# Kernel optimization log

Measured on AMD Instinct MI355X. Metric: run time of the kernel, lower is better.

## Reference

```python
import jax, jax.numpy as jnp
import numpy as np

NUM_HEADS = 16


def setup_inputs() -> dict:
    key = jax.random.key(0)
    ks = jax.random.split(key, 11)
    S, E, F = 4096, 2048, 8192
    s = lambda k, shape, fan_in: jax.random.normal(k, shape, jnp.float32) / np.sqrt(fan_in)
    return {
        "emb": jax.random.normal(ks[0], (S, E), jnp.float32),
        "Wq": s(ks[1], (E, E), E), "bq": jnp.zeros((E,), jnp.float32),
        "Wk": s(ks[2], (E, E), E), "bk": jnp.zeros((E,), jnp.float32),
        "Wv": s(ks[3], (E, E), E), "bv": jnp.zeros((E,), jnp.float32),
        "W1": s(ks[4], (E, F), E), "b1": jnp.zeros((F,), jnp.float32),
        "W2": s(ks[5], (F, E), F), "b2": jnp.zeros((E,), jnp.float32),
    }


def reference(emb, Wq, bq, Wk, bk, Wv, bv, W1, b1, W2, b2):
    S, E = emb.shape
    H = NUM_HEADS
    D = E // H
    # project and split heads -> [H, S, D]
    q = (emb @ Wq + bq).reshape(S, H, D).transpose(1, 0, 2)
    k = (emb @ Wk + bk).reshape(S, H, D).transpose(1, 0, 2)
    v = (emb @ Wv + bv).reshape(S, H, D).transpose(1, 0, 2)
    scale = jnp.asarray(D, emb.dtype) ** 0.5
    scores = jnp.einsum("hsd,htd->hst", q, k) / scale  # [H, S, S]
    # causal mask: additive -1e9 strictly above the diagonal (matches torch.triu(..., 1)*-1e9)
    mask = jnp.triu(jnp.full((S, S), -1e9, dtype=scores.dtype), k=1)
    probs = jax.nn.softmax(scores + mask, axis=-1)
    attn = jnp.einsum("hst,htd->hsd", probs, v)  # [H, S, D]
    attn = attn.transpose(1, 0, 2).reshape(S, E)  # concat heads -> [S, E]
    hidden = jnp.maximum(attn @ W1 + b1, 0.0)
    return hidden @ W2 + b2
```

## Files before the change

### kernel.cpp

```cpp
#include <hip/hip_runtime.h>

typedef __attribute__((ext_vector_type(8))) short bf16x8;
typedef __attribute__((ext_vector_type(4))) float f32x4;
typedef __attribute__((ext_vector_type(8))) unsigned short u16x8;

static constexpr int S = 4096;
static constexpr int E = 2048;
static constexpr int F = 8192;
static constexpr int NH = 16;
static constexpr int DH = 128;

__device__ __forceinline__ unsigned short f2bf(float f) {
  unsigned u = __builtin_bit_cast(unsigned, f);
  u += 0x7FFFu + ((u >> 16) & 1u);
  return (unsigned short)(u >> 16);
}

__device__ __forceinline__ void async16(const unsigned short* g, unsigned short* l) {
  __builtin_amdgcn_global_load_lds(
      (const __attribute__((address_space(1))) unsigned int*)g,
      (__attribute__((address_space(3))) unsigned int*)l, 16, 0, 0);
}

__global__ __launch_bounds__(256) void cvt_bf16_kernel(const float* __restrict__ src,
                                                       unsigned short* __restrict__ dst) {
  int i = (blockIdx.x * 256 + threadIdx.x) * 4;
  float4 v = *(const float4*)(src + i);
  ushort4 o;
  o.x = f2bf(v.x); o.y = f2bf(v.y); o.z = f2bf(v.z); o.w = f2bf(v.w);
  *(ushort4*)(dst + i) = o;
}

__global__ __launch_bounds__(256) void transpose_cvt(const float* __restrict__ src,
                                                     unsigned short* __restrict__ dst,
                                                     const int Rr, const int Cc) {
  __shared__ float t[32][33];
  const int c0 = blockIdx.x * 32, r0 = blockIdx.y * 32;
  const int tx = threadIdx.x, ty = threadIdx.y;
#pragma unroll
  for (int i = 0; i < 4; ++i) {
    int r = ty + i * 8;
    t[r][tx] = src[(size_t)(r0 + r) * Cc + c0 + tx];
  }
  __syncthreads();
#pragma unroll
  for (int i = 0; i < 4; ++i) {
    int cr = ty + i * 8;
    dst[(size_t)(c0 + cr) * Rr + r0 + tx] = f2bf(t[tx][cr]);
  }
}

enum { EPI_QKV = 0, EPI_RELU = 1, EPI_OUT = 2 };

template <int EPI>
__global__ __launch_bounds__(256) void gemm_bt(
    const unsigned short* __restrict__ A, const unsigned short* __restrict__ B,
    const int K, const int N,
    const float* __restrict__ b0, const float* __restrict__ b1f, const float* __restrict__ b2f,
    unsigned short* __restrict__ o0, unsigned short* __restrict__ o1,
    unsigned short* __restrict__ o2, float* __restrict__ of) {
  __shared__ unsigned short lA[2][128 * 32];
  __shared__ unsigned short lB[2][128 * 32];
  const int tid = threadIdx.x, w = tid >> 6, lane = tid & 63;
  const int lane15 = lane & 15, l4 = lane >> 4;
  const int m0 = blockIdx.y * 128, n0 = blockIdx.x * 128;
  const int wr = w >> 1, wc = w & 1;

  const int u0 = (w * 2 + 0) * 64 + lane;
  const int u1 = (w * 2 + 1) * 64 + lane;
  const unsigned short* gA0 = A + (size_t)(m0 + (u0 >> 2)) * K + (u0 & 3) * 8;
  const unsigned short* gA1 = A + (size_t)(m0 + (u1 >> 2)) * K + (u1 & 3) * 8;
  const unsigned short* gB0 = B + (size_t)(n0 + (u0 >> 2)) * K + (u0 & 3) * 8;
  const unsigned short* gB1 = B + (size_t)(n0 + (u1 >> 2)) * K + (u1 & 3) * 8;
  const int doff0 = (w * 2 + 0) * 512;
  const int doff1 = (w * 2 + 1) * 512;

  f32x4 zero4 = {0.f, 0.f, 0.f, 0.f};
  f32x4 acc[4][4];
#pragma unroll
  for (int i = 0; i < 4; ++i)
#pragma unroll
    for (int j = 0; j < 4; ++j) acc[i][j] = zero4;

  async16(gA0, &lA[0][doff0]);
  async16(gA1, &lA[0][doff1]);
  async16(gB0, &lB[0][doff0]);
  async16(gB1, &lB[0][doff1]);

  for (int ko = 0; ko < K; ko += 32) {
    __syncthreads();
    const int buf = (ko >> 5) & 1;
    if (ko + 32 < K) {
      const int nb = buf ^ 1;
      async16(gA0 + ko + 32, &lA[nb][doff0]);
      async16(gA1 + ko + 32, &lA[nb][doff1]);
      async16(gB0 + ko + 32, &lB[nb][doff0]);
      async16(gB1 + ko + 32, &lB[nb][doff1]);
    }
    bf16x8 av[4], bv[4];
#pragma unroll
    for (int i = 0; i < 4; ++i)
      av[i] = *(const bf16x8*)&lA[buf][(wr * 64 + i * 16 + lane15) * 32 + l4 * 8];
#pragma unroll
    for (int j = 0; j < 4; ++j)
      bv[j] = *(const bf16x8*)&lB[buf][(wc * 64 + j * 16 + lane15) * 32 + l4 * 8];
#pragma unroll
    for (int i = 0; i < 4; ++i)
#pragma unroll
      for (int j = 0; j < 4; ++j)
        acc[i][j] = __builtin_amdgcn_mfma_f32_16x16x32_bf16(av[i], bv[j], acc[i][j], 0, 0, 0);
  }

#pragma unroll
  for (int j = 0; j < 4; ++j) {
    const int n = n0 + wc * 64 + j * 16 + lane15;
    float bias;
    if (EPI == EPI_QKV)
      bias = (n < E) ? b0[n] : ((n < 2 * E) ? b1f[n - E] : b2f[n - 2 * E]);
    else
      bias = b0[n];
#pragma unroll
    for (int i = 0; i < 4; ++i) {
      const int mr = m0 + wr * 64 + i * 16 + l4 * 4;
      f32x4 v = acc[i][j];
#pragma unroll
      for (int r = 0; r < 4; ++r) {
        const float val = v[r] + bias;
        const int m = mr + r;
        if (EPI == EPI_QKV) {
          if (n < E)            o0[(size_t)m * E + n] = f2bf(val);
          else if (n < 2 * E)   o1[(size_t)m * E + (n - E)] = f2bf(val);
          else                  o2[(size_t)(n - 2 * E) * S + m] = f2bf(val);
        } else if (EPI == EPI_RELU) {
          o0[(size_t)m * N + n] = f2bf(fmaxf(val, 0.f));
        } else {
          of[(size_t)m * N + n] = val;
        }
      }
    }
  }
}

__global__ __launch_bounds__(256, 2) void flash_attn(const unsigned short* __restrict__ Qb,
                                                     const unsigned short* __restrict__ Kb,
                                                     const unsigned short* __restrict__ VTb,
                                                     unsigned short* __restrict__ attn) {
  const int qt = gridDim.x - 1 - blockIdx.x;
  const int h = blockIdx.y;
  const int qbase = qt * 64;
  const int tid = threadIdx.x, w = tid >> 6, lane = tid & 63;
  const int lane15 = lane & 15, l4 = lane >> 4;

  __shared__ unsigned short lK[2][64 * 128];
  __shared__ unsigned short lV[2][128 * 64];
  __shared__ unsigned short lP[4][16 * 72];

  bf16x8 aq[4];
  {
    const unsigned short* qrow = Qb + (size_t)(qbase + w * 16 + lane15) * E + h * DH + l4 * 8;
#pragma unroll
    for (int kk = 0; kk < 4; ++kk) aq[kk] = *(const bf16x8*)(qrow + kk * 32);
  }

  f32x4 zero4 = {0.f, 0.f, 0.f, 0.f};
  f32x4 o[8];
  float psum[4];
#pragma unroll
  for (int j = 0; j < 8; ++j) o[j] = zero4;
#pragma unroll
  for (int r = 0; r < 4; ++r) psum[r] = 0.f;

  {
#pragma unroll
    for (int i = 0; i < 4; ++i) {
      int c = i * 256 + w * 64 + lane;
      int row = c >> 4, pg = (c & 15) ^ (row & 15);
      async16(Kb + (size_t)row * E + h * DH + pg * 8, &lK[0][(i * 256 + w * 64) * 8]);
    }
#pragma unroll
    for (int i = 0; i < 4; ++i) {
      int c = i * 256 + w * 64 + lane;
      int row = c >> 3, pg = (c & 7) ^ (row & 7);
      async16(VTb + (size_t)(h * DH + row) * S + pg * 8, &lV[0][(i * 256 + w * 64) * 8]);
    }
  }

  const float scale = 0.088388347648318447f;

  for (int kt = 0; kt <= qt; ++kt) {
    __syncthreads();
    if (kt < qt) {
      const int kb2 = (kt + 1) * 64;
      const int nb = (kt + 1) & 1;
#pragma unroll
      for (int i = 0; i < 4; ++i) {
        int c = i * 256 + w * 64 + lane;
        int row = c >> 4, pg = (c & 15) ^ (row & 15);
        async16(Kb + (size_t)(kb2 + row) * E + h * DH + pg * 8, &lK[nb][(i * 256 + w * 64) * 8]);
      }
#pragma unroll
      for (int i = 0; i < 4; ++i) {
        int c = i * 256 + w * 64 + lane;
        int row = c >> 3, pg = (c & 7) ^ (row & 7);
        async16(VTb + (size_t)(h * DH + row) * S + kb2 + pg * 8, &lV[nb][(i * 256 + w * 64) * 8]);
      }
    }
    const int buf = kt & 1;

    f32x4 sacc[4];
#pragma unroll
    for (int j = 0; j < 4; ++j) sacc[j] = zero4;
#pragma unroll
    for (int kk = 0; kk < 4; ++kk)
#pragma unroll
      for (int j = 0; j < 4; ++j) {
        int pl = (kk * 4 + l4) ^ lane15;
        bf16x8 bk = *(const bf16x8*)&lK[buf][(j * 16 + lane15) * 128 + pl * 8];
        sacc[j] = __builtin_amdgcn_mfma_f32_16x16x32_bf16(aq[kk], bk, sacc[j], 0, 0, 0);
      }

    float p[4][4];
    if (kt == qt) {
#pragma unroll
      for (int j = 0; j < 4; ++j) {
        int col = j * 16 + lane15;
#pragma unroll
        for (int r = 0; r < 4; ++r) {
          int row = w * 16 + l4 * 4 + r;
          p[j][r] = (col <= row) ? __expf(sacc[j][r] * scale) : 0.f;
        }
      }
    } else {
#pragma unroll
      for (int j = 0; j < 4; ++j)
#pragma unroll
        for (int r = 0; r < 4; ++r) p[j][r] = __expf(sacc[j][r] * scale);
    }
#pragma unroll
    for (int r = 0; r < 4; ++r) psum[r] += p[0][r] + p[1][r] + p[2][r] + p[3][r];

#pragma unroll
    for (int j = 0; j < 4; ++j)
#pragma unroll
      for (int r = 0; r < 4; ++r)
        lP[w][(l4 * 4 + r) * 72 + j * 16 + lane15] = f2bf(p[j][r]);

#pragma unroll
    for (int ks = 0; ks < 2; ++ks) {
      bf16x8 ap = *(const bf16x8*)&lP[w][lane15 * 72 + ks * 32 + l4 * 8];
#pragma unroll
      for (int j = 0; j < 8; ++j) {
        int pl = (ks * 4 + l4) ^ (lane15 & 7);
        bf16x8 bv = *(const bf16x8*)&lV[buf][(j * 16 + lane15) * 64 + pl * 8];
        o[j] = __builtin_amdgcn_mfma_f32_16x16x32_bf16(ap, bv, o[j], 0, 0, 0);
      }
    }
  }

  float inv[4];
#pragma unroll
  for (int r = 0; r < 4; ++r) {
    float s = psum[r];
#pragma unroll
    for (int off = 1; off < 16; off <<= 1) s += __shfl_xor(s, off, 16);
    inv[r] = 1.0f / s;
  }
#pragma unroll
  for (int j = 0; j < 8; ++j)
#pragma unroll
    for (int r = 0; r < 4; ++r)
      attn[(size_t)(qbase + w * 16 + l4 * 4 + r) * E + h * DH + j * 16 + lane15] =
          f2bf(o[j][r] * inv[r]);
}

extern "C" void kernel_launch(void* const* d_in, const int* in_sizes, int n_in,
                              void* d_out, int out_size, void* d_ws, size_t ws_size,
                              hipStream_t stream) {
  (void)in_sizes; (void)n_in; (void)out_size; (void)ws_size;
  const float* emb = (const float*)d_in[0];
  const float* Wq  = (const float*)d_in[1];
  const float* bq  = (const float*)d_in[2];
  const float* Wk  = (const float*)d_in[3];
  const float* bk  = (const float*)d_in[4];
  const float* Wv  = (const float*)d_in[5];
  const float* bv  = (const float*)d_in[6];
  const float* W1  = (const float*)d_in[7];
  const float* b1  = (const float*)d_in[8];
  const float* W2  = (const float*)d_in[9];
  const float* b2  = (const float*)d_in[10];
  float* out = (float*)d_out;

  char* ws = (char*)d_ws;
  const size_t MB = 1024ull * 1024ull;
  unsigned short* embb   = (unsigned short*)(ws);
  unsigned short* attn   = embb;
  char* r1 = ws + 16 * MB;
  unsigned short* WqkvT  = (unsigned short*)(r1);
  unsigned short* Qb     = (unsigned short*)(r1 + 24 * MB);
  unsigned short* Kb     = (unsigned short*)(r1 + 40 * MB);
  unsigned short* VTb    = (unsigned short*)(r1 + 56 * MB);
  unsigned short* hidden = (unsigned short*)(r1);
  unsigned short* W1T    = (unsigned short*)(r1 + 72 * MB);
  unsigned short* W2T    = (unsigned short*)(r1 + 104 * MB);

  dim3 b256(256);
  dim3 tb(32, 8);
  cvt_bf16_kernel<<<dim3((S * E) / 1024), b256, 0, stream>>>(emb, embb);
  transpose_cvt<<<dim3(E / 32, E / 32), tb, 0, stream>>>(Wq, WqkvT, E, E);
  transpose_cvt<<<dim3(E / 32, E / 32), tb, 0, stream>>>(Wk, WqkvT + (size_t)E * E, E, E);
  transpose_cvt<<<dim3(E / 32, E / 32), tb, 0, stream>>>(Wv, WqkvT + 2ull * E * E, E, E);
  transpose_cvt<<<dim3(F / 32, E / 32), tb, 0, stream>>>(W1, W1T, E, F);
  transpose_cvt<<<dim3(E / 32, F / 32), tb, 0, stream>>>(W2, W2T, F, E);

  gemm_bt<EPI_QKV><<<dim3(3 * E / 128, S / 128), b256, 0, stream>>>(
      embb, WqkvT, E, 3 * E, bq, bk, bv, Qb, Kb, VTb, nullptr);
  flash_attn<<<dim3(S / 64, NH), b256, 0, stream>>>(Qb, Kb, VTb, attn);
  gemm_bt<EPI_RELU><<<dim3(F / 128, S / 128), b256, 0, stream>>>(
      attn, W1T, E, F, b1, nullptr, nullptr, hidden, nullptr, nullptr, nullptr);
  gemm_bt<EPI_OUT><<<dim3(E / 128, S / 128), b256, 0, stream>>>(
      hidden, W2T, F, E, b2, nullptr, nullptr, nullptr, nullptr, nullptr, out);
}
```

Before: 915.9 us.

## Process 128 query rows per attention block with two row groups per wave

```diff
diff --git a/kernel.cpp b/kernel.cpp
--- a/kernel.cpp
+++ b/kernel.cpp
@@ -145,30 +145,36 @@
                                                      const unsigned short* __restrict__ Kb,
                                                      const unsigned short* __restrict__ VTb,
                                                      unsigned short* __restrict__ attn) {
-  const int qt = gridDim.x - 1 - blockIdx.x;
+  const int x = blockIdx.x;
   const int h = blockIdx.y;
-  const int qbase = qt * 64;
+  const int qt = (h < 8) ? (31 - x) : x;
+  const int qbase = qt * 128;
   const int tid = threadIdx.x, w = tid >> 6, lane = tid & 63;
   const int lane15 = lane & 15, l4 = lane >> 4;
+  const int rowb = qbase + w * 32;
 
   __shared__ unsigned short lK[2][64 * 128];
   __shared__ unsigned short lV[2][128 * 64];
   __shared__ unsigned short lP[4][16 * 72];
 
-  bf16x8 aq[4];
-  {
-    const unsigned short* qrow = Qb + (size_t)(qbase + w * 16 + lane15) * E + h * DH + l4 * 8;
-#pragma unroll
-    for (int kk = 0; kk < 4; ++kk) aq[kk] = *(const bf16x8*)(qrow + kk * 32);
+  bf16x8 aq[2][4];
+#pragma unroll
+  for (int rg = 0; rg < 2; ++rg) {
+    const unsigned short* qrow = Qb + (size_t)(rowb + rg * 16 + lane15) * E + h * DH + l4 * 8;
+#pragma unroll
+    for (int kk = 0; kk < 4; ++kk) aq[rg][kk] = *(const bf16x8*)(qrow + kk * 32);
   }
 
   f32x4 zero4 = {0.f, 0.f, 0.f, 0.f};
-  f32x4 o[8];
-  float psum[4];
-#pragma unroll
-  for (int j = 0; j < 8; ++j) o[j] = zero4;
-#pragma unroll
-  for (int r = 0; r < 4; ++r) psum[r] = 0.f;
+  f32x4 o[2][8];
+  float psum[2][4];
+#pragma unroll
+  for (int rg = 0; rg < 2; ++rg) {
+#pragma unroll
+    for (int j = 0; j < 8; ++j) o[rg][j] = zero4;
+#pragma unroll
+    for (int r = 0; r < 4; ++r) psum[rg][r] = 0.f;
+  }
 
   {
 #pragma unroll
@@ -186,10 +192,11 @@
   }
 
   const float scale = 0.088388347648318447f;
-
-  for (int kt = 0; kt <= qt; ++kt) {
+  const int ktmax = 2 * qt + 1;
+
+  for (int kt = 0; kt <= ktmax; ++kt) {
     __syncthreads();
-    if (kt < qt) {
+    if (kt < ktmax) {
       const int kb2 = (kt + 1) * 64;
       const int nb = (kt + 1) & 1;
 #pragma unroll
@@ -205,72 +212,87 @@
         async16(VTb + (size_t)(h * DH + row) * S + kb2 + pg * 8, &lV[nb][(i * 256 + w * 64) * 8]);
       }
     }
+    if (kt * 64 > rowb + 31) continue;
     const int buf = kt & 1;
 
-    f32x4 sacc[4];
-#pragma unroll
-    for (int j = 0; j < 4; ++j) sacc[j] = zero4;
+    f32x4 sacc[2][4];
+#pragma unroll
+    for (int rg = 0; rg < 2; ++rg)
+#pragma unroll
+      for (int j = 0; j < 4; ++j) sacc[rg][j] = zero4;
 #pragma unroll
     for (int kk = 0; kk < 4; ++kk)
 #pragma unroll
       for (int j = 0; j < 4; ++j) {
         int pl = (kk * 4 + l4) ^ lane15;
         bf16x8 bk = *(const bf16x8*)&lK[buf][(j * 16 + lane15) * 128 + pl * 8];
-        sacc[j] = __builtin_amdgcn_mfma_f32_16x16x32_bf16(aq[kk], bk, sacc[j], 0, 0, 0);
-      }
-
-    float p[4][4];
-    if (kt == qt) {
-#pragma unroll
-      for (int j = 0; j < 4; ++j) {
-        int col = j * 16 + lane15;
-#pragma unroll
-        for (int r = 0; r < 4; ++r) {
-          int row = w * 16 + l4 * 4 + r;
-          p[j][r] = (col <= row) ? __expf(sacc[j][r] * scale) : 0.f;
+        sacc[0][j] = __builtin_amdgcn_mfma_f32_16x16x32_bf16(aq[0][kk], bk, sacc[0][j], 0, 0, 0);
+        sacc[1][j] = __builtin_amdgcn_mfma_f32_16x16x32_bf16(aq[1][kk], bk, sacc[1][j], 0, 0, 0);
+      }
+
+    const bool diag = (kt * 64 + 63 > rowb);
+    bf16x8 ap[2][2];
+#pragma unroll
+    for (int rg = 0; rg < 2; ++rg) {
+      float p[4][4];
+      if (diag) {
+#pragma unroll
+        for (int j = 0; j < 4; ++j) {
+          int col = kt * 64 + j * 16 + lane15;
+#pragma unroll
+          for (int r = 0; r < 4; ++r) {
+            int row = rowb + rg * 16 + l4 * 4 + r;
+            p[j][r] = (col <= row) ? __expf(sacc[rg][j][r] * scale) : 0.f;
+          }
         }
-      }
-    } else {
+      } else {
+#pragma unroll
+        for (int j = 0; j < 4; ++j)
+#pragma unroll
+          for (int r = 0; r < 4; ++r) p[j][r] = __expf(sacc[rg][j][r] * scale);
+      }
+#pragma unroll
+      for (int r = 0; r < 4; ++r) psum[rg][r] += p[0][r] + p[1][r] + p[2][r] + p[3][r];
+
 #pragma unroll
       for (int j = 0; j < 4; ++j)
 #pragma unroll
-        for (int r = 0; r < 4; ++r) p[j][r] = __expf(sacc[j][r] * scale);
-    }
-#pragma unroll
-    for (int r = 0; r < 4; ++r) psum[r] += p[0][r] + p[1][r] + p[2][r] + p[3][r];
-
-#pragma unroll
-    for (int j = 0; j < 4; ++j)
-#pragma unroll
-      for (int r = 0; r < 4; ++r)
-        lP[w][(l4 * 4 + r) * 72 + j * 16 + lane15] = f2bf(p[j][r]);
-
-#pragma unroll
-    for (int ks = 0; ks < 2; ++ks) {
-      bf16x8 ap = *(const bf16x8*)&lP[w][lane15 * 72 + ks * 32 + l4 * 8];
+        for (int r = 0; r < 4; ++r)
+          lP[w][(l4 * 4 + r) * 72 + j * 16 + lane15] = f2bf(p[j][r]);
+
+#pragma unroll
+      for (int ks = 0; ks < 2; ++ks)
+        ap[rg][ks] = *(const bf16x8*)&lP[w][lane15 * 72 + ks * 32 + l4 * 8];
+    }
+
+#pragma unroll
+    for (int ks = 0; ks < 2; ++ks)
 #pragma unroll
       for (int j = 0; j < 8; ++j) {
         int pl = (ks * 4 + l4) ^ (lane15 & 7);
         bf16x8 bv = *(const bf16x8*)&lV[buf][(j * 16 + lane15) * 64 + pl * 8];
-        o[j] = __builtin_amdgcn_mfma_f32_16x16x32_bf16(ap, bv, o[j], 0, 0, 0);
-      }
-    }
-  }
-
-  float inv[4];
-#pragma unroll
-  for (int r = 0; r < 4; ++r) {
-    float s = psum[r];
-#pragma unroll
-    for (int off = 1; off < 16; off <<= 1) s += __shfl_xor(s, off, 16);
-    inv[r] = 1.0f / s;
-  }
-#pragma unroll
-  for (int j = 0; j < 8; ++j)
-#pragma unroll
-    for (int r = 0; r < 4; ++r)
-      attn[(size_t)(qbase + w * 16 + l4 * 4 + r) * E + h * DH + j * 16 + lane15] =
-          f2bf(o[j][r] * inv[r]);
+        o[0][j] = __builtin_amdgcn_mfma_f32_16x16x32_bf16(ap[0][ks], bv, o[0][j], 0, 0, 0);
+        o[1][j] = __builtin_amdgcn_mfma_f32_16x16x32_bf16(ap[1][ks], bv, o[1][j], 0, 0, 0);
+      }
+  }
+
+#pragma unroll
+  for (int rg = 0; rg < 2; ++rg) {
+    float inv[4];
+#pragma unroll
+    for (int r = 0; r < 4; ++r) {
+      float s = psum[rg][r];
+#pragma unroll
+      for (int off = 1; off < 16; off <<= 1) s += __shfl_xor(s, off, 16);
+      inv[r] = 1.0f / s;
+    }
+#pragma unroll
+    for (int j = 0; j < 8; ++j)
+#pragma unroll
+      for (int r = 0; r < 4; ++r)
+        attn[(size_t)(rowb + rg * 16 + l4 * 4 + r) * E + h * DH + j * 16 + lane15] =
+            f2bf(o[rg][j][r] * inv[r]);
+  }
 }
 
 extern "C" void kernel_launch(void* const* d_in, const int* in_sizes, int n_in,
@@ -314,7 +336,7 @@
 
   gemm_bt<EPI_QKV><<<dim3(3 * E / 128, S / 128), b256, 0, stream>>>(
       embb, WqkvT, E, 3 * E, bq, bk, bv, Qb, Kb, VTb, nullptr);
-  flash_attn<<<dim3(S / 64, NH), b256, 0, stream>>>(Qb, Kb, VTb, attn);
+  flash_attn<<<dim3(S / 128, NH), b256, 0, stream>>>(Qb, Kb, VTb, attn);
   gemm_bt<EPI_RELU><<<dim3(F / 128, S / 128), b256, 0, stream>>>(
       attn, W1T, E, F, b1, nullptr, nullptr, hidden, nullptr, nullptr, nullptr);
   gemm_bt<EPI_OUT><<<dim3(E / 128, S / 128), b256, 0, stream>>>(
```

New measurement: 852.3 us. 1.07x faster.
